# Performance work log

Hardware: AMD Instinct MI355X
Metric: run time of the kernel (lower is better)

## Reference

```python
import jax, jax.numpy as jnp
import numpy as np

B, N, E = 2, 5000, 160000
F_IN, HID, ED = 128, 128, 16
IN_EDGE = 2 * F_IN + 16 + ED  # source, target, radial(4*4), edge_attr


def _lin(k, fan_in, fan_out):
    return (jax.random.normal(k, (fan_in, fan_out), jnp.float32) / np.sqrt(fan_in)).astype(jnp.float32)


def setup_inputs() -> dict:
    key = jax.random.key(0)
    ks = jax.random.split(key, 16)
    h = jax.random.normal(ks[0], (B, N, F_IN), jnp.float32)
    coord = jax.random.normal(ks[1], (B, N, 4, 3), jnp.float32)
    edge_index = jax.random.randint(ks[2], (2, E), 0, N)
    edge_attr = jax.random.normal(ks[3], (E, ED), jnp.float32)
    return {
        "h": h, "coord": coord, "edge_index": edge_index, "edge_attr": edge_attr,
        # edge_mlp: Linear(IN_EDGE->HID), ReLU, Linear(HID->HID), ReLU
        "W_e1": _lin(ks[4], IN_EDGE, HID), "b_e1": jnp.zeros((HID,), jnp.float32),
        "W_e2": _lin(ks[5], HID, HID), "b_e2": jnp.zeros((HID,), jnp.float32),
        # node_mlp: Linear(HID+F_IN->HID), ReLU, Linear(HID->F_IN)
        "W_n1": _lin(ks[6], HID + F_IN, HID), "b_n1": jnp.zeros((HID,), jnp.float32),
        "W_n2": _lin(ks[7], HID, F_IN), "b_n2": jnp.zeros((F_IN,), jnp.float32),
        # coord_mlp: Linear(HID->HID), ReLU, Linear(HID->4, bias=False, xavier gain 0.001)
        "W_c1": _lin(ks[8], HID, HID), "b_c1": jnp.zeros((HID,), jnp.float32),
        "W_c2": _lin(ks[9], HID, 4) * 0.001,
    }


def reference(h, coord, edge_index, edge_attr,
              W_e1, b_e1, W_e2, b_e2,
              W_n1, b_n1, W_n2, b_n2,
              W_c1, b_c1, W_c2):
    row, col = edge_index[0], edge_index[1]
    coords_weight = 1.0
    n_nodes = h.shape[1]

    def single(h_b, coord_b):
        # coord2radial
        cd = coord_b[row] - coord_b[col]                                  # [E,4,3]
        prod = jnp.einsum('ejt,ekt->ejk', cd, cd).reshape(cd.shape[0], -1)  # [E,16]
        nrm = jnp.linalg.norm(prod, axis=-1, keepdims=True)
        radial = prod / jnp.maximum(nrm, 1e-12)                           # F.normalize
        # edge_model
        x = jnp.concatenate([h_b[row], h_b[col], radial, edge_attr], axis=-1)
        ef = jax.nn.relu(jax.nn.relu(x @ W_e1 + b_e1) @ W_e2 + b_e2)      # [E,HID]
        # coord_model: segment mean of cd * coord_mlp(ef)
        w = jax.nn.relu(ef @ W_c1 + b_c1) @ W_c2                          # [E,4]
        trans = cd * w[:, :, None]                                        # [E,4,3]
        agg_c = jax.ops.segment_sum(trans, row, num_segments=n_nodes)     # [N,4,3]
        cnt = jax.ops.segment_sum(jnp.ones((row.shape[0],), trans.dtype), row,
                                  num_segments=n_nodes)                   # [N]
        coord_new = coord_b + (agg_c / jnp.maximum(cnt, 1.0)[:, None, None]) * coords_weight
        # node_model (recurrent)
        agg_h = jax.ops.segment_sum(ef, row, num_segments=n_nodes)        # [N,HID]
        z = jnp.concatenate([h_b, agg_h], axis=-1)
        h_new = h_b + jax.nn.relu(z @ W_n1 + b_n1) @ W_n2 + b_n2
        return h_new, coord_new

    hs, coords = jax.vmap(single)(h, coord)
    return hs, coords
```

## Files before the change

### kernel.cpp

```cpp
#include <hip/hip_runtime.h>
#include <hip/hip_bf16.h>

#define B   2
#define NN_ 5000
#define NE_ 160000
#define F   128
#define HID 128
#define ED  16

typedef __bf16 bf16x8 __attribute__((ext_vector_type(8)));
typedef __bf16 bf16x4 __attribute__((ext_vector_type(4)));
typedef float  f32x4  __attribute__((ext_vector_type(4)));

#define MS  136
#define PS  40
#define EDG 64
#define ZS  264
#define HS  136
#define NPB2 32
#define NBUCKET 313

__global__ void pack_weights(const float* __restrict__ We1, const float* __restrict__ We2,
                             const float* __restrict__ Wc1, const float* __restrict__ Wc2,
                             const float* __restrict__ Wn1, const float* __restrict__ Wn2,
                             __bf16* __restrict__ pw1, __bf16* __restrict__ pw2,
                             __bf16* __restrict__ pwc1, __bf16* __restrict__ pwc2,
                             __bf16* __restrict__ pwn1, __bf16* __restrict__ pwn2,
                             float4* __restrict__ agg4, int* __restrict__ csr_cnt)
{
    int idx = blockIdx.x * 256 + threadIdx.x;
    const float* W; __bf16* P; int KT, Nr, local;
    if (idx < 36864)       { W = We1; P = pw1;  KT = 9; Nr = 128; local = idx; }
    else if (idx < 53248)  { W = We2; P = pw2;  KT = 4; Nr = 128; local = idx - 36864; }
    else if (idx < 69632)  { W = Wc1; P = pwc1; KT = 4; Nr = 128; local = idx - 53248; }
    else if (idx < 71680)  { W = Wc2; P = pwc2; KT = 4; Nr = 4;   local = idx - 69632; }
    else if (idx < 104448) { W = Wn1; P = pwn1; KT = 8; Nr = 128; local = idx - 71680; }
    else                   { W = Wn2; P = pwn2; KT = 4; Nr = 128; local = idx - 104448; }
    int j = local & 7, lane = (local >> 3) & 63, rest = local >> 9;
    int kt = rest % KT, nt = rest / KT;
    int k = kt * 32 + (lane >> 4) * 8 + j;
    int n = nt * 16 + (lane & 15);
    float v = (n < Nr) ? W[k * Nr + n] : 0.f;
    P[local] = (__bf16)v;

    float4 z4 = {0.f, 0.f, 0.f, 0.f};
    for (int i = idx; i < 350000; i += 120832) agg4[i] = z4;
    if (idx < NN_) csr_cnt[idx] = 0;
}

__global__ void hist_kernel(const int* __restrict__ ei, int* __restrict__ csr_cnt)
{
    int i = blockIdx.x * 256 + threadIdx.x;
    if (i < NE_) atomicAdd(&csr_cnt[ei[i]], 1);
}

__global__ void scan_kernel(const int* __restrict__ csr_cnt,
                            int* __restrict__ csr_off, int* __restrict__ csr_pos)
{
    __shared__ int part[256];
    const int t = threadIdx.x;
    int sum = 0;
    #pragma unroll
    for (int j = 0; j < 20; j++) {
        int idx = t * 20 + j;
        if (idx < NN_) sum += csr_cnt[idx];
    }
    part[t] = sum;
    __syncthreads();
    if (t == 0) {
        int run = 0;
        for (int i = 0; i < 256; i++) { int v = part[i]; part[i] = run; run += v; }
    }
    __syncthreads();
    int run = part[t];
    #pragma unroll
    for (int j = 0; j < 20; j++) {
        int idx = t * 20 + j;
        if (idx < NN_) { csr_off[idx] = run; csr_pos[idx] = run; run += csr_cnt[idx]; }
    }
    if (t == 0) csr_off[NN_] = NE_;
}

__global__ __launch_bounds__(512) void mid_kernel(
    const int* __restrict__ ei, const float* __restrict__ ea,
    int* __restrict__ csr_pos, int* __restrict__ bucket, __bf16* __restrict__ eas,
    const float* __restrict__ h, const __bf16* __restrict__ pw1,
    __bf16* __restrict__ pr, __bf16* __restrict__ pc)
{
    __shared__ __align__(16) __bf16 hs[128 * MS];
    const int t = threadIdx.x;

    if (blockIdx.x < NBUCKET) {
        int i = blockIdx.x * 512 + t;
        if (i < NE_) {
            int p = atomicAdd(&csr_pos[ei[i]], 1);
            bucket[p] = i;
            const float4* src = (const float4*)(ea + (size_t)i * ED);
            __bf16* dst = eas + (size_t)p * ED;
            #pragma unroll
            for (int j = 0; j < 4; j++) {
                float4 v = src[j];
                bf16x4 bv = {(__bf16)v.x, (__bf16)v.y, (__bf16)v.z, (__bf16)v.w};
                *(bf16x4*)&dst[j * 4] = bv;
            }
        }
        return;
    }

    const int bp = blockIdx.x - NBUCKET;
    const int b = bp / 40;
    const int n0 = (bp % 40) * 128;
    const int lane = t & 63, wave = t >> 6;
    const int quad = lane >> 4, c = lane & 15;

    #pragma unroll
    for (int it = 0; it < 8; it++) {
        int idx = it * 512 + t;
        int node = idx >> 5, ch = idx & 31;
        int gn = n0 + node;
        float4 v = (gn < NN_) ? *(const float4*)&h[((size_t)b * NN_ + gn) * F + ch * 4]
                              : (float4){0.f, 0.f, 0.f, 0.f};
        bf16x4 bv = {(__bf16)v.x, (__bf16)v.y, (__bf16)v.z, (__bf16)v.w};
        *(bf16x4*)&hs[node * MS + ch * 4] = bv;
    }
    __syncthreads();

    const bf16x8* pw1v = (const bf16x8*)pw1;
    f32x4 accr[8], accc[8];
    #pragma unroll
    for (int m = 0; m < 8; m++) { accr[m] = (f32x4){0,0,0,0}; accc[m] = (f32x4){0,0,0,0}; }
    for (int kt = 0; kt < 4; kt++) {
        bf16x8 wr = pw1v[(wave * 9 + kt) * 64 + lane];
        bf16x8 wc = pw1v[(wave * 9 + kt + 4) * 64 + lane];
        #pragma unroll
        for (int m = 0; m < 8; m++) {
            bf16x8 x = *(const bf16x8*)&hs[(m * 16 + c) * MS + kt * 32 + quad * 8];
            accr[m] = __builtin_amdgcn_mfma_f32_16x16x32_bf16(wr, x, accr[m], 0, 0, 0);
            accc[m] = __builtin_amdgcn_mfma_f32_16x16x32_bf16(wc, x, accc[m], 0, 0, 0);
        }
    }
    #pragma unroll
    for (int m = 0; m < 8; m++) {
        int gn = n0 + m * 16 + c;
        if (gn < NN_) {
            size_t base = ((size_t)b * NN_ + gn) * F + wave * 16 + quad * 4;
            bf16x4 orr = {(__bf16)accr[m][0], (__bf16)accr[m][1], (__bf16)accr[m][2], (__bf16)accr[m][3]};
            bf16x4 occ = {(__bf16)accc[m][0], (__bf16)accc[m][1], (__bf16)accc[m][2], (__bf16)accc[m][3]};
            *(bf16x4*)&pr[base] = orr;
            *(bf16x4*)&pc[base] = occ;
        }
    }
}

__global__ __launch_bounds__(256, 4) void edge_kernel(
    const __bf16* __restrict__ pr, const __bf16* __restrict__ pc,
    const float* __restrict__ coord,
    const int* __restrict__ ei, const __bf16* __restrict__ eas,
    const int* __restrict__ bucket,
    const float* __restrict__ be1, const float* __restrict__ be2,
    const float* __restrict__ bc1,
    const __bf16* __restrict__ pw1, const __bf16* __restrict__ pw2,
    const __bf16* __restrict__ pwc1, const __bf16* __restrict__ pwc2,
    float* __restrict__ agg_h, float* __restrict__ agg_c)
{
    __shared__ __align__(16) __bf16 buf1[EDG * MS];
    __shared__ __align__(16) __bf16 buf2[EDG * MS];
    __shared__ __bf16 cds[EDG][12];
    __shared__ int rs[EDG], cs[EDG];

    const int t = threadIdx.x;
    const int b = blockIdx.y;
    const int p0 = blockIdx.x * EDG;
    const int lane = t & 63, wave = t >> 6;
    const int quad = lane >> 4, c = lane & 15;

    if (t < EDG) {
        int eid = bucket[p0 + t];
        rs[t] = ei[eid]; cs[t] = ei[NE_ + eid];
    }
    __syncthreads();

    const __bf16* prb = pr + (size_t)b * NN_ * F;
    const __bf16* pcb = pc + (size_t)b * NN_ * F;
    #pragma unroll
    for (int it = 0; it < 4; it++) {
        int idx = it * 256 + t;
        int e = idx >> 4, ch = idx & 15;
        bf16x8 a = *(const bf16x8*)(prb + (size_t)rs[e] * F + ch * 8);
        bf16x8 v = *(const bf16x8*)(pcb + (size_t)cs[e] * F + ch * 8);
        bf16x8 o;
        #pragma unroll
        for (int j = 0; j < 8; j++) o[j] = (__bf16)((float)a[j] + (float)v[j]);
        *(bf16x8*)&buf1[e * MS + ch * 8] = o;
    }
    if (t < EDG) {
        int e = t;
        const float* cr = coord + ((size_t)b * NN_ + rs[e]) * 12;
        const float* cc = coord + ((size_t)b * NN_ + cs[e]) * 12;
        float cd[12];
        #pragma unroll
        for (int j = 0; j < 12; j++) { cd[j] = cr[j] - cc[j]; cds[e][j] = (__bf16)cd[j]; }
        float prod[16]; float ss = 0.f;
        #pragma unroll
        for (int j = 0; j < 4; j++)
            #pragma unroll
            for (int k = 0; k < 4; k++) {
                float p = cd[j*3]*cd[k*3] + cd[j*3+1]*cd[k*3+1] + cd[j*3+2]*cd[k*3+2];
                prod[j*4 + k] = p; ss += p * p;
            }
        float inv = 1.0f / fmaxf(sqrtf(ss), 1e-12f);
        #pragma unroll
        for (int j = 0; j < 16; j++) buf2[e * PS + j] = (__bf16)(prod[j] * inv);
        const uint4* ep = (const uint4*)(eas + (size_t)(p0 + e) * 16);
        *(uint4*)&buf2[e * PS + 16] = ep[0];
        *(uint4*)&buf2[e * PS + 24] = ep[1];
    }
    __syncthreads();

    const bf16x8* pw1v  = (const bf16x8*)pw1;
    const bf16x8* pw2v  = (const bf16x8*)pw2;
    const bf16x8* pwc1v = (const bf16x8*)pwc1;
    const bf16x8* pwc2v = (const bf16x8*)pwc2;

    f32x4 acc1[4][2];
    #pragma unroll
    for (int m = 0; m < 4; m++)
        #pragma unroll
        for (int n = 0; n < 2; n++) acc1[m][n] = (f32x4){0,0,0,0};
    {
        bf16x8 x1[4];
        #pragma unroll
        for (int m = 0; m < 4; m++)
            x1[m] = *(const bf16x8*)&buf2[(m*16 + c) * PS + quad*8];
        #pragma unroll
        for (int n = 0; n < 2; n++) {
            bf16x8 w = pw1v[((2*wave + n)*9 + 8)*64 + lane];
            #pragma unroll
            for (int m = 0; m < 4; m++)
                acc1[m][n] = __builtin_amdgcn_mfma_f32_16x16x32_bf16(w, x1[m], acc1[m][n], 0, 0, 0);
        }
    }
    #pragma unroll
    for (int n = 0; n < 2; n++) {
        int nt = 2*wave + n;
        float4 bb = *(const float4*)&be1[nt*16 + quad*4];
        #pragma unroll
        for (int m = 0; m < 4; m++) {
            int row = m*16 + c;
            bf16x4 p = *(const bf16x4*)&buf1[row * MS + nt*16 + quad*4];
            bf16x4 o = { (__bf16)fmaxf(acc1[m][n][0] + (float)p[0] + bb.x, 0.f),
                         (__bf16)fmaxf(acc1[m][n][1] + (float)p[1] + bb.y, 0.f),
                         (__bf16)fmaxf(acc1[m][n][2] + (float)p[2] + bb.z, 0.f),
                         (__bf16)fmaxf(acc1[m][n][3] + (float)p[3] + bb.w, 0.f) };
            *(bf16x4*)&buf1[row * MS + nt*16 + quad*4] = o;
        }
    }
    __syncthreads();

    f32x4 acc2[4][2];
    #pragma unroll
    for (int m = 0; m < 4; m++)
        #pragma unroll
        for (int n = 0; n < 2; n++) acc2[m][n] = (f32x4){0,0,0,0};
    for (int kt = 0; kt < 4; kt++) {
        bf16x8 x[4];
        #pragma unroll
        for (int m = 0; m < 4; m++)
            x[m] = *(const bf16x8*)&buf1[(m*16 + c) * MS + kt*32 + quad*8];
        #pragma unroll
        for (int n = 0; n < 2; n++) {
            bf16x8 w = pw2v[((2*wave + n)*4 + kt)*64 + lane];
            #pragma unroll
            for (int m = 0; m < 4; m++)
                acc2[m][n] = __builtin_amdgcn_mfma_f32_16x16x32_bf16(w, x[m], acc2[m][n], 0, 0, 0);
        }
    }
    #pragma unroll
    for (int n = 0; n < 2; n++) {
        int nt = 2*wave + n;
        float4 bb = *(const float4*)&be2[nt*16 + quad*4];
        #pragma unroll
        for (int m = 0; m < 4; m++) {
            int row = m*16 + c;
            bf16x4 o = { (__bf16)fmaxf(acc2[m][n][0] + bb.x, 0.f),
                         (__bf16)fmaxf(acc2[m][n][1] + bb.y, 0.f),
                         (__bf16)fmaxf(acc2[m][n][2] + bb.z, 0.f),
                         (__bf16)fmaxf(acc2[m][n][3] + bb.w, 0.f) };
            *(bf16x4*)&buf2[row * MS + nt*16 + quad*4] = o;
        }
    }
    __syncthreads();

    f32x4 acc3[4][2];
    #pragma unroll
    for (int m = 0; m < 4; m++)
        #pragma unroll
        for (int n = 0; n < 2; n++) acc3[m][n] = (f32x4){0,0,0,0};
    for (int kt = 0; kt < 4; kt++) {
        bf16x8 x[4];
        #pragma unroll
        for (int m = 0; m < 4; m++)
            x[m] = *(const bf16x8*)&buf2[(m*16 + c) * MS + kt*32 + quad*8];
        #pragma unroll
        for (int n = 0; n < 2; n++) {
            bf16x8 w = pwc1v[((2*wave + n)*4 + kt)*64 + lane];
            #pragma unroll
            for (int m = 0; m < 4; m++)
                acc3[m][n] = __builtin_amdgcn_mfma_f32_16x16x32_bf16(w, x[m], acc3[m][n], 0, 0, 0);
        }
    }
    #pragma unroll
    for (int n = 0; n < 2; n++) {
        int nt = 2*wave + n;
        float4 bb = *(const float4*)&bc1[nt*16 + quad*4];
        #pragma unroll
        for (int m = 0; m < 4; m++) {
            int row = m*16 + c;
            bf16x4 o = { (__bf16)fmaxf(acc3[m][n][0] + bb.x, 0.f),
                         (__bf16)fmaxf(acc3[m][n][1] + bb.y, 0.f),
                         (__bf16)fmaxf(acc3[m][n][2] + bb.z, 0.f),
                         (__bf16)fmaxf(acc3[m][n][3] + bb.w, 0.f) };
            *(bf16x4*)&buf1[row * MS + nt*16 + quad*4] = o;
        }
    }
    __syncthreads();

    f32x4 accw = (f32x4){0,0,0,0};
    for (int kt = 0; kt < 4; kt++) {
        bf16x8 x = *(const bf16x8*)&buf1[(wave*16 + c) * MS + kt*32 + quad*8];
        accw = __builtin_amdgcn_mfma_f32_16x16x32_bf16(pwc2v[kt*64 + lane], x, accw, 0, 0, 0);
    }
    if (quad == 0) {
        int e = wave*16 + c;
        #pragma unroll
        for (int j = 0; j < 12; j++)
            cds[e][j] = (__bf16)((float)cds[e][j] * accw[j/3]);
    }
    __syncthreads();

    {
        float* aggh_b = agg_h + (size_t)b * NN_ * HID;
        const int cp = t & 63;
        const int seg = t >> 6;
        float r0 = 0.f, r1 = 0.f;
        int cur = rs[seg * 16];
        for (int e = seg * 16; e < seg * 16 + 16; e++) {
            int r = rs[e];
            unsigned u = *(const unsigned*)&buf2[e * MS + cp * 2];
            float v0 = __uint_as_float(u << 16);
            float v1 = __uint_as_float(u & 0xffff0000u);
            if (r != cur) {
                atomicAdd(&aggh_b[(size_t)cur * HID + cp*2],     r0);
                atomicAdd(&aggh_b[(size_t)cur * HID + cp*2 + 1], r1);
                r0 = r1 = 0.f; cur = r;
            }
            r0 += v0; r1 += v1;
        }
        atomicAdd(&aggh_b[(size_t)cur * HID + cp*2],     r0);
        atomicAdd(&aggh_b[(size_t)cur * HID + cp*2 + 1], r1);
    }
    if (t < 48) {
        float* aggc_b = agg_c + (size_t)b * NN_ * 12;
        const int j = t % 12, q = t / 12;
        float run = 0.f;
        int cur = rs[q * 16];
        for (int e = q * 16; e < q * 16 + 16; e++) {
            int r = rs[e];
            float v = (float)cds[e][j];
            if (r != cur) {
                atomicAdd(&aggc_b[(size_t)cur * 12 + j], run);
                run = 0.f; cur = r;
            }
            run += v;
        }
        atomicAdd(&aggc_b[(size_t)cur * 12 + j], run);
    }
}

__global__ __launch_bounds__(256) void node_kernel(
    const float* __restrict__ h, const float* __restrict__ agg_h,
    const float* __restrict__ agg_c, const float* __restrict__ coord,
    const int* __restrict__ csr_off,
    const __bf16* __restrict__ pwn1, const float* __restrict__ bn1,
    const __bf16* __restrict__ pwn2, const float* __restrict__ bn2,
    float* __restrict__ out_h, float* __restrict__ out_c)
{
    __shared__ __align__(16) __bf16 zs[NPB2 * ZS];
    __shared__ __align__(16) __bf16 h1s[NPB2 * HS];
    const int t = threadIdx.x;
    const int b = blockIdx.y;
    const int n0 = blockIdx.x * NPB2;
    const int lane = t & 63, wave = t >> 6;
    const int quad = lane >> 4, c = lane & 15;

    #pragma unroll
    for (int it = 0; it < 8; it++) {
        int idx = it * 256 + t;
        int node = idx >> 6, ch = idx & 63;
        int gn = n0 + node;
        float4 v = (float4){0.f, 0.f, 0.f, 0.f};
        if (gn < NN_) {
            const float* src = (ch < 32) ? &h[((size_t)b * NN_ + gn) * F + ch * 4]
                                         : &agg_h[((size_t)b * NN_ + gn) * HID + (ch - 32) * 4];
            v = *(const float4*)src;
        }
        bf16x4 bv = {(__bf16)v.x, (__bf16)v.y, (__bf16)v.z, (__bf16)v.w};
        *(bf16x4*)&zs[node * ZS + ch * 4] = bv;
    }
    __syncthreads();

    const bf16x8* w1v = (const bf16x8*)pwn1;
    const bf16x8* w2v = (const bf16x8*)pwn2;
    f32x4 a1[2][2];
    #pragma unroll
    for (int m = 0; m < 2; m++)
        #pragma unroll
        for (int n = 0; n < 2; n++) a1[m][n] = (f32x4){0,0,0,0};
    for (int kt = 0; kt < 8; kt++) {
        bf16x8 x[2];
        #pragma unroll
        for (int m = 0; m < 2; m++)
            x[m] = *(const bf16x8*)&zs[(m*16 + c) * ZS + kt*32 + quad*8];
        #pragma unroll
        for (int n = 0; n < 2; n++) {
            bf16x8 w = w1v[((2*wave + n)*8 + kt)*64 + lane];
            #pragma unroll
            for (int m = 0; m < 2; m++)
                a1[m][n] = __builtin_amdgcn_mfma_f32_16x16x32_bf16(w, x[m], a1[m][n], 0, 0, 0);
        }
    }
    __syncthreads();
    #pragma unroll
    for (int n = 0; n < 2; n++) {
        int nt = 2*wave + n;
        float4 bb = *(const float4*)&bn1[nt*16 + quad*4];
        #pragma unroll
        for (int m = 0; m < 2; m++) {
            bf16x4 o = { (__bf16)fmaxf(a1[m][n][0] + bb.x, 0.f),
                         (__bf16)fmaxf(a1[m][n][1] + bb.y, 0.f),
                         (__bf16)fmaxf(a1[m][n][2] + bb.z, 0.f),
                         (__bf16)fmaxf(a1[m][n][3] + bb.w, 0.f) };
            *(bf16x4*)&h1s[(m*16 + c) * HS + nt*16 + quad*4] = o;
        }
    }
    __syncthreads();

    f32x4 a2[2][2];
    #pragma unroll
    for (int m = 0; m < 2; m++)
        #pragma unroll
        for (int n = 0; n < 2; n++) a2[m][n] = (f32x4){0,0,0,0};
    for (int kt = 0; kt < 4; kt++) {
        bf16x8 x[2];
        #pragma unroll
        for (int m = 0; m < 2; m++)
            x[m] = *(const bf16x8*)&h1s[(m*16 + c) * HS + kt*32 + quad*8];
        #pragma unroll
        for (int n = 0; n < 2; n++) {
            bf16x8 w = w2v[((2*wave + n)*4 + kt)*64 + lane];
            #pragma unroll
            for (int m = 0; m < 2; m++)
                a2[m][n] = __builtin_amdgcn_mfma_f32_16x16x32_bf16(w, x[m], a2[m][n], 0, 0, 0);
        }
    }
    float* os = (float*)zs;
    #pragma unroll
    for (int n = 0; n < 2; n++) {
        int nt = 2*wave + n;
        float4 bb = *(const float4*)&bn2[nt*16 + quad*4];
        #pragma unroll
        for (int m = 0; m < 2; m++) {
            f32x4 o = { a2[m][n][0] + bb.x, a2[m][n][1] + bb.y,
                        a2[m][n][2] + bb.z, a2[m][n][3] + bb.w };
            *(f32x4*)&os[(m*16 + c) * 132 + nt*16 + quad*4] = o;
        }
    }
    __syncthreads();

    #pragma unroll
    for (int it = 0; it < 4; it++) {
        int idx = it * 256 + t;
        int node = idx >> 5, ch = idx & 31;
        int gn = n0 + node;
        if (gn < NN_) {
            size_t gb = ((size_t)b * NN_ + gn) * F + ch * 4;
            float4 hres = *(const float4*)&h[gb];
            float4 acc = *(const float4*)&os[node * 132 + ch * 4];
            float4 o = { hres.x + acc.x, hres.y + acc.y, hres.z + acc.z, hres.w + acc.w };
            *(float4*)&out_h[gb] = o;
        }
    }
    for (int idx = t; idx < NPB2 * 12; idx += 256) {
        int node = idx / 12, j = idx % 12;
        int gn = n0 + node;
        if (gn < NN_) {
            float deg = (float)(csr_off[gn + 1] - csr_off[gn]);
            size_t ci = ((size_t)b * NN_ + gn) * 12 + j;
            out_c[ci] = coord[ci] + agg_c[ci] / fmaxf(deg, 1.0f);
        }
    }
}

extern "C" void kernel_launch(void* const* d_in, const int* in_sizes, int n_in,
                              void* d_out, int out_size, void* d_ws, size_t ws_size,
                              hipStream_t stream) {
    const float* h     = (const float*)d_in[0];
    const float* coord = (const float*)d_in[1];
    const int*   ei    = (const int*)d_in[2];
    const float* ea    = (const float*)d_in[3];
    const float* We1   = (const float*)d_in[4];
    const float* be1   = (const float*)d_in[5];
    const float* We2   = (const float*)d_in[6];
    const float* be2   = (const float*)d_in[7];
    const float* Wn1   = (const float*)d_in[8];
    const float* bn1   = (const float*)d_in[9];
    const float* Wn2   = (const float*)d_in[10];
    const float* bn2   = (const float*)d_in[11];
    const float* Wc1   = (const float*)d_in[12];
    const float* bc1   = (const float*)d_in[13];
    const float* Wc2   = (const float*)d_in[14];

    float* out_h = (float*)d_out;
    float* out_c = out_h + (size_t)B * NN_ * F;

    unsigned char* base = (unsigned char*)d_ws;
    __bf16* pw1  = (__bf16*)base;
    __bf16* pw2  = pw1 + 36864;
    __bf16* pwc1 = pw2 + 16384;
    __bf16* pwc2 = pwc1 + 16384;
    __bf16* pwn1 = pwc2 + 2048;
    __bf16* pwn2 = pwn1 + 32768;
    unsigned char* dyn = base + 241664;

    int* csr_cnt = (int*)(dyn);
    int* csr_off = (int*)(dyn + 20000);
    int* csr_pos = (int*)(dyn + 40016);
    int* bucket  = (int*)(dyn + 60016);
    float* agg_h = (float*)(dyn + 700016);
    float* agg_c = agg_h + (size_t)B * NN_ * HID;
    __bf16* pr   = (__bf16*)(agg_c + (size_t)B * NN_ * 12);
    __bf16* pc   = pr + (size_t)B * NN_ * F;
    __bf16* eas  = pc + (size_t)B * NN_ * F;

    pack_weights<<<472, 256, 0, stream>>>(We1, We2, Wc1, Wc2, Wn1, Wn2,
                                          pw1, pw2, pwc1, pwc2, pwn1, pwn2,
                                          (float4*)agg_h, csr_cnt);

    hist_kernel<<<625, 256, 0, stream>>>(ei, csr_cnt);
    scan_kernel<<<1, 256, 0, stream>>>(csr_cnt, csr_off, csr_pos);

    mid_kernel<<<NBUCKET + 80, 512, 0, stream>>>(ei, ea, csr_pos, bucket, eas,
                                                 h, pw1, pr, pc);

    dim3 eg(NE_ / EDG, B);
    edge_kernel<<<eg, 256, 0, stream>>>(pr, pc, coord, ei, eas, bucket, be1, be2, bc1,
                                        pw1, pw2, pwc1, pwc2, agg_h, agg_c);

    dim3 ng((NN_ + NPB2 - 1) / NPB2, B);
    node_kernel<<<ng, 256, 0, stream>>>(h, agg_h, agg_c, coord, csr_off,
                                        pwn1, bn1, pwn2, bn2, out_h, out_c);
}
```

Before: 204.1 us.

## Merge setup kernels into one cooperative kernel; gather projections into registers

The four setup launches (weight packing, histogram, scan, bucket plus node projection) become one cooperative kernel of 256 blocks that uses grid-wide syncs between phases, and the scan becomes a parallel Hillis-Steele pass. The goal is to remove launch gaps and tail idling between small kernels. In the edge kernel, the projected row and column features are now loaded straight into registers in MFMA output layout, so the shared-memory staging pass and its barrier are gone. An extra __syncthreads is added, and the grid syncs plus the fixed grid size could limit parallelism in the bucket and projection phases.

```diff
diff --git a/kernel.cpp b/kernel.cpp
--- a/kernel.cpp
+++ b/kernel.cpp
@@ -1,5 +1,8 @@
 #include <hip/hip_runtime.h>
 #include <hip/hip_bf16.h>
+#include <hip/hip_cooperative_groups.h>
+
+namespace cg = cooperative_groups;
 
 #define B   2
 #define NN_ 5000
@@ -18,136 +21,133 @@
 #define ZS  264
 #define HS  136
 #define NPB2 32
-#define NBUCKET 313
-
-__global__ void pack_weights(const float* __restrict__ We1, const float* __restrict__ We2,
-                             const float* __restrict__ Wc1, const float* __restrict__ Wc2,
-                             const float* __restrict__ Wn1, const float* __restrict__ Wn2,
-                             __bf16* __restrict__ pw1, __bf16* __restrict__ pw2,
-                             __bf16* __restrict__ pwc1, __bf16* __restrict__ pwc2,
-                             __bf16* __restrict__ pwn1, __bf16* __restrict__ pwn2,
-                             float4* __restrict__ agg4, int* __restrict__ csr_cnt)
-{
-    int idx = blockIdx.x * 256 + threadIdx.x;
-    const float* W; __bf16* P; int KT, Nr, local;
-    if (idx < 36864)       { W = We1; P = pw1;  KT = 9; Nr = 128; local = idx; }
-    else if (idx < 53248)  { W = We2; P = pw2;  KT = 4; Nr = 128; local = idx - 36864; }
-    else if (idx < 69632)  { W = Wc1; P = pwc1; KT = 4; Nr = 128; local = idx - 53248; }
-    else if (idx < 71680)  { W = Wc2; P = pwc2; KT = 4; Nr = 4;   local = idx - 69632; }
-    else if (idx < 104448) { W = Wn1; P = pwn1; KT = 8; Nr = 128; local = idx - 71680; }
-    else                   { W = Wn2; P = pwn2; KT = 4; Nr = 128; local = idx - 104448; }
-    int j = local & 7, lane = (local >> 3) & 63, rest = local >> 9;
-    int kt = rest % KT, nt = rest / KT;
-    int k = kt * 32 + (lane >> 4) * 8 + j;
-    int n = nt * 16 + (lane & 15);
-    float v = (n < Nr) ? W[k * Nr + n] : 0.f;
-    P[local] = (__bf16)v;
-
-    float4 z4 = {0.f, 0.f, 0.f, 0.f};
-    for (int i = idx; i < 350000; i += 120832) agg4[i] = z4;
-    if (idx < NN_) csr_cnt[idx] = 0;
-}
-
-__global__ void hist_kernel(const int* __restrict__ ei, int* __restrict__ csr_cnt)
-{
-    int i = blockIdx.x * 256 + threadIdx.x;
-    if (i < NE_) atomicAdd(&csr_cnt[ei[i]], 1);
-}
-
-__global__ void scan_kernel(const int* __restrict__ csr_cnt,
-                            int* __restrict__ csr_off, int* __restrict__ csr_pos)
-{
-    __shared__ int part[256];
-    const int t = threadIdx.x;
-    int sum = 0;
-    #pragma unroll
-    for (int j = 0; j < 20; j++) {
-        int idx = t * 20 + j;
-        if (idx < NN_) sum += csr_cnt[idx];
-    }
-    part[t] = sum;
-    __syncthreads();
-    if (t == 0) {
-        int run = 0;
-        for (int i = 0; i < 256; i++) { int v = part[i]; part[i] = run; run += v; }
-    }
-    __syncthreads();
-    int run = part[t];
-    #pragma unroll
-    for (int j = 0; j < 20; j++) {
-        int idx = t * 20 + j;
-        if (idx < NN_) { csr_off[idx] = run; csr_pos[idx] = run; run += csr_cnt[idx]; }
-    }
-    if (t == 0) csr_off[NN_] = NE_;
-}
-
-__global__ __launch_bounds__(512) void mid_kernel(
+
+__global__ __launch_bounds__(512) void setup_kernel(
+    const float* __restrict__ We1, const float* __restrict__ We2,
+    const float* __restrict__ Wc1, const float* __restrict__ Wc2,
+    const float* __restrict__ Wn1, const float* __restrict__ Wn2,
     const int* __restrict__ ei, const float* __restrict__ ea,
-    int* __restrict__ csr_pos, int* __restrict__ bucket, __bf16* __restrict__ eas,
-    const float* __restrict__ h, const __bf16* __restrict__ pw1,
+    const float* __restrict__ h,
+    __bf16* __restrict__ pw1, __bf16* __restrict__ pw2,
+    __bf16* __restrict__ pwc1, __bf16* __restrict__ pwc2,
+    __bf16* __restrict__ pwn1, __bf16* __restrict__ pwn2,
+    float4* __restrict__ agg4, int* __restrict__ csr_cnt,
+    int* __restrict__ csr_off, int* __restrict__ csr_pos,
+    int* __restrict__ bucket, __bf16* __restrict__ eas,
     __bf16* __restrict__ pr, __bf16* __restrict__ pc)
 {
     __shared__ __align__(16) __bf16 hs[128 * MS];
+    __shared__ int part[512];
+    cg::grid_group grid = cg::this_grid();
     const int t = threadIdx.x;
-
-    if (blockIdx.x < NBUCKET) {
-        int i = blockIdx.x * 512 + t;
-        if (i < NE_) {
-            int p = atomicAdd(&csr_pos[ei[i]], 1);
-            bucket[p] = i;
-            const float4* src = (const float4*)(ea + (size_t)i * ED);
-            __bf16* dst = eas + (size_t)p * ED;
-            #pragma unroll
-            for (int j = 0; j < 4; j++) {
-                float4 v = src[j];
-                bf16x4 bv = {(__bf16)v.x, (__bf16)v.y, (__bf16)v.z, (__bf16)v.w};
-                *(bf16x4*)&dst[j * 4] = bv;
+    const int gid = blockIdx.x * 512 + t;
+
+    if (gid < 120832) {
+        int idx = gid;
+        const float* W; __bf16* P; int KT, Nr, local;
+        if (idx < 36864)       { W = We1; P = pw1;  KT = 9; Nr = 128; local = idx; }
+        else if (idx < 53248)  { W = We2; P = pw2;  KT = 4; Nr = 128; local = idx - 36864; }
+        else if (idx < 69632)  { W = Wc1; P = pwc1; KT = 4; Nr = 128; local = idx - 53248; }
+        else if (idx < 71680)  { W = Wc2; P = pwc2; KT = 4; Nr = 4;   local = idx - 69632; }
+        else if (idx < 104448) { W = Wn1; P = pwn1; KT = 8; Nr = 128; local = idx - 71680; }
+        else                   { W = Wn2; P = pwn2; KT = 4; Nr = 128; local = idx - 104448; }
+        int j = local & 7, lane = (local >> 3) & 63, rest = local >> 9;
+        int kt = rest % KT, nt = rest / KT;
+        int k = kt * 32 + (lane >> 4) * 8 + j;
+        int n = nt * 16 + (lane & 15);
+        float v = (n < Nr) ? W[k * Nr + n] : 0.f;
+        P[local] = (__bf16)v;
+    }
+    {
+        float4 z4 = {0.f, 0.f, 0.f, 0.f};
+        for (int i = gid; i < 350000; i += 131072) agg4[i] = z4;
+    }
+    if (gid < NN_) csr_cnt[gid] = 0;
+    grid.sync();
+
+    for (int i = gid; i < NE_; i += 131072) atomicAdd(&csr_cnt[ei[i]], 1);
+    grid.sync();
+
+    if (blockIdx.x == 0) {
+        int sum = 0;
+        #pragma unroll
+        for (int j = 0; j < 10; j++) {
+            int idx = t * 10 + j;
+            if (idx < NN_) sum += csr_cnt[idx];
+        }
+        part[t] = sum;
+        __syncthreads();
+        for (int off = 1; off < 512; off <<= 1) {
+            int v = (t >= off) ? part[t - off] : 0;
+            __syncthreads();
+            part[t] += v;
+            __syncthreads();
+        }
+        int run = part[t] - sum;
+        #pragma unroll
+        for (int j = 0; j < 10; j++) {
+            int idx = t * 10 + j;
+            if (idx < NN_) { csr_off[idx] = run; csr_pos[idx] = run; run += csr_cnt[idx]; }
+        }
+        if (t == 0) csr_off[NN_] = NE_;
+    }
+    grid.sync();
+
+    for (int i = gid; i < NE_; i += 131072) {
+        int p = atomicAdd(&csr_pos[ei[i]], 1);
+        bucket[p] = i;
+        const float4* src = (const float4*)(ea + (size_t)i * ED);
+        __bf16* dst = eas + (size_t)p * ED;
+        #pragma unroll
+        for (int j = 0; j < 4; j++) {
+            float4 v = src[j];
+            bf16x4 bv = {(__bf16)v.x, (__bf16)v.y, (__bf16)v.z, (__bf16)v.w};
+            *(bf16x4*)&dst[j * 4] = bv;
+        }
+    }
+    if (blockIdx.x >= 176) {
+        const int bp = blockIdx.x - 176;
+        const int b = bp / 40;
+        const int n0 = (bp % 40) * 128;
+        const int lane = t & 63, wave = t >> 6;
+        const int quad = lane >> 4, c = lane & 15;
+
+        #pragma unroll
+        for (int it = 0; it < 8; it++) {
+            int idx = it * 512 + t;
+            int node = idx >> 5, ch = idx & 31;
+            int gn = n0 + node;
+            float4 v = (gn < NN_) ? *(const float4*)&h[((size_t)b * NN_ + gn) * F + ch * 4]
+                                  : (float4){0.f, 0.f, 0.f, 0.f};
+            bf16x4 bv = {(__bf16)v.x, (__bf16)v.y, (__bf16)v.z, (__bf16)v.w};
+            *(bf16x4*)&hs[node * MS + ch * 4] = bv;
+        }
+        __syncthreads();
+
+        const bf16x8* pw1v = (const bf16x8*)pw1;
+        f32x4 accr[8], accc[8];
+        #pragma unroll
+        for (int m = 0; m < 8; m++) { accr[m] = (f32x4){0,0,0,0}; accc[m] = (f32x4){0,0,0,0}; }
+        for (int kt = 0; kt < 4; kt++) {
+            bf16x8 wr = pw1v[(wave * 9 + kt) * 64 + lane];
+            bf16x8 wc = pw1v[(wave * 9 + kt + 4) * 64 + lane];
+            #pragma unroll
+            for (int m = 0; m < 8; m++) {
+                bf16x8 x = *(const bf16x8*)&hs[(m * 16 + c) * MS + kt * 32 + quad * 8];
+                accr[m] = __builtin_amdgcn_mfma_f32_16x16x32_bf16(wr, x, accr[m], 0, 0, 0);
+                accc[m] = __builtin_amdgcn_mfma_f32_16x16x32_bf16(wc, x, accc[m], 0, 0, 0);
             }
         }
-        return;
-    }
-
-    const int bp = blockIdx.x - NBUCKET;
-    const int b = bp / 40;
-    const int n0 = (bp % 40) * 128;
-    const int lane = t & 63, wave = t >> 6;
-    const int quad = lane >> 4, c = lane & 15;
-
-    #pragma unroll
-    for (int it = 0; it < 8; it++) {
-        int idx = it * 512 + t;
-        int node = idx >> 5, ch = idx & 31;
-        int gn = n0 + node;
-        float4 v = (gn < NN_) ? *(const float4*)&h[((size_t)b * NN_ + gn) * F + ch * 4]
-                              : (float4){0.f, 0.f, 0.f, 0.f};
-        bf16x4 bv = {(__bf16)v.x, (__bf16)v.y, (__bf16)v.z, (__bf16)v.w};
-        *(bf16x4*)&hs[node * MS + ch * 4] = bv;
-    }
-    __syncthreads();
-
-    const bf16x8* pw1v = (const bf16x8*)pw1;
-    f32x4 accr[8], accc[8];
-    #pragma unroll
-    for (int m = 0; m < 8; m++) { accr[m] = (f32x4){0,0,0,0}; accc[m] = (f32x4){0,0,0,0}; }
-    for (int kt = 0; kt < 4; kt++) {
-        bf16x8 wr = pw1v[(wave * 9 + kt) * 64 + lane];
-        bf16x8 wc = pw1v[(wave * 9 + kt + 4) * 64 + lane];
         #pragma unroll
         for (int m = 0; m < 8; m++) {
-            bf16x8 x = *(const bf16x8*)&hs[(m * 16 + c) * MS + kt * 32 + quad * 8];
-            accr[m] = __builtin_amdgcn_mfma_f32_16x16x32_bf16(wr, x, accr[m], 0, 0, 0);
-            accc[m] = __builtin_amdgcn_mfma_f32_16x16x32_bf16(wc, x, accc[m], 0, 0, 0);
-        }
-    }
-    #pragma unroll
-    for (int m = 0; m < 8; m++) {
-        int gn = n0 + m * 16 + c;
-        if (gn < NN_) {
-            size_t base = ((size_t)b * NN_ + gn) * F + wave * 16 + quad * 4;
-            bf16x4 orr = {(__bf16)accr[m][0], (__bf16)accr[m][1], (__bf16)accr[m][2], (__bf16)accr[m][3]};
-            bf16x4 occ = {(__bf16)accc[m][0], (__bf16)accc[m][1], (__bf16)accc[m][2], (__bf16)accc[m][3]};
-            *(bf16x4*)&pr[base] = orr;
-            *(bf16x4*)&pc[base] = occ;
+            int gn = n0 + m * 16 + c;
+            if (gn < NN_) {
+                size_t base = ((size_t)b * NN_ + gn) * F + wave * 16 + quad * 4;
+                bf16x4 orr = {(__bf16)accr[m][0], (__bf16)accr[m][1], (__bf16)accr[m][2], (__bf16)accr[m][3]};
+                bf16x4 occ = {(__bf16)accc[m][0], (__bf16)accc[m][1], (__bf16)accc[m][2], (__bf16)accc[m][3]};
+                *(bf16x4*)&pr[base] = orr;
+                *(bf16x4*)&pc[base] = occ;
+            }
         }
     }
 }
@@ -175,28 +175,12 @@
     const int quad = lane >> 4, c = lane & 15;
 
     if (t < EDG) {
-        int eid = bucket[p0 + t];
-        rs[t] = ei[eid]; cs[t] = ei[NE_ + eid];
-    }
-    __syncthreads();
-
-    const __bf16* prb = pr + (size_t)b * NN_ * F;
-    const __bf16* pcb = pc + (size_t)b * NN_ * F;
-    #pragma unroll
-    for (int it = 0; it < 4; it++) {
-        int idx = it * 256 + t;
-        int e = idx >> 4, ch = idx & 15;
-        bf16x8 a = *(const bf16x8*)(prb + (size_t)rs[e] * F + ch * 8);
-        bf16x8 v = *(const bf16x8*)(pcb + (size_t)cs[e] * F + ch * 8);
-        bf16x8 o;
-        #pragma unroll
-        for (int j = 0; j < 8; j++) o[j] = (__bf16)((float)a[j] + (float)v[j]);
-        *(bf16x8*)&buf1[e * MS + ch * 8] = o;
-    }
-    if (t < EDG) {
         int e = t;
-        const float* cr = coord + ((size_t)b * NN_ + rs[e]) * 12;
-        const float* cc = coord + ((size_t)b * NN_ + cs[e]) * 12;
+        int eid = bucket[p0 + e];
+        int r = ei[eid], cl = ei[NE_ + eid];
+        rs[e] = r; cs[e] = cl;
+        const float* cr = coord + ((size_t)b * NN_ + r) * 12;
+        const float* cc = coord + ((size_t)b * NN_ + cl) * 12;
         float cd[12];
         #pragma unroll
         for (int j = 0; j < 12; j++) { cd[j] = cr[j] - cc[j]; cds[e][j] = (__bf16)cd[j]; }
@@ -221,6 +205,20 @@
     const bf16x8* pw2v  = (const bf16x8*)pw2;
     const bf16x8* pwc1v = (const bf16x8*)pwc1;
     const bf16x8* pwc2v = (const bf16x8*)pwc2;
+    const __bf16* prb = pr + (size_t)b * NN_ * F;
+    const __bf16* pcb = pc + (size_t)b * NN_ * F;
+
+    bf16x4 pgr[2][4], pgc[2][4];
+    #pragma unroll
+    for (int n = 0; n < 2; n++) {
+        int fo = (2*wave + n)*16 + quad*4;
+        #pragma unroll
+        for (int m = 0; m < 4; m++) {
+            int e = m*16 + c;
+            pgr[n][m] = *(const bf16x4*)(prb + (size_t)rs[e] * F + fo);
+            pgc[n][m] = *(const bf16x4*)(pcb + (size_t)cs[e] * F + fo);
+        }
+    }
 
     f32x4 acc1[4][2];
     #pragma unroll
@@ -247,11 +245,10 @@
         #pragma unroll
         for (int m = 0; m < 4; m++) {
             int row = m*16 + c;
-            bf16x4 p = *(const bf16x4*)&buf1[row * MS + nt*16 + quad*4];
-            bf16x4 o = { (__bf16)fmaxf(acc1[m][n][0] + (float)p[0] + bb.x, 0.f),
-                         (__bf16)fmaxf(acc1[m][n][1] + (float)p[1] + bb.y, 0.f),
-                         (__bf16)fmaxf(acc1[m][n][2] + (float)p[2] + bb.z, 0.f),
-                         (__bf16)fmaxf(acc1[m][n][3] + (float)p[3] + bb.w, 0.f) };
+            bf16x4 o = { (__bf16)fmaxf(acc1[m][n][0] + (float)pgr[n][m][0] + (float)pgc[n][m][0] + bb.x, 0.f),
+                         (__bf16)fmaxf(acc1[m][n][1] + (float)pgr[n][m][1] + (float)pgc[n][m][1] + bb.y, 0.f),
+                         (__bf16)fmaxf(acc1[m][n][2] + (float)pgr[n][m][2] + (float)pgc[n][m][2] + bb.z, 0.f),
+                         (__bf16)fmaxf(acc1[m][n][3] + (float)pgr[n][m][3] + (float)pgc[n][m][3] + bb.w, 0.f) };
             *(bf16x4*)&buf1[row * MS + nt*16 + quad*4] = o;
         }
     }
@@ -275,6 +272,7 @@
                 acc2[m][n] = __builtin_amdgcn_mfma_f32_16x16x32_bf16(w, x[m], acc2[m][n], 0, 0, 0);
         }
     }
+    __syncthreads();
     #pragma unroll
     for (int n = 0; n < 2; n++) {
         int nt = 2*wave + n;
@@ -542,15 +540,15 @@
     __bf16* pc   = pr + (size_t)B * NN_ * F;
     __bf16* eas  = pc + (size_t)B * NN_ * F;
 
-    pack_weights<<<472, 256, 0, stream>>>(We1, We2, Wc1, Wc2, Wn1, Wn2,
-                                          pw1, pw2, pwc1, pwc2, pwn1, pwn2,
-                                          (float4*)agg_h, csr_cnt);
-
-    hist_kernel<<<625, 256, 0, stream>>>(ei, csr_cnt);
-    scan_kernel<<<1, 256, 0, stream>>>(csr_cnt, csr_off, csr_pos);
-
-    mid_kernel<<<NBUCKET + 80, 512, 0, stream>>>(ei, ea, csr_pos, bucket, eas,
-                                                 h, pw1, pr, pc);
+    float4* agg4 = (float4*)agg_h;
+    void* args[] = {
+        (void*)&We1, (void*)&We2, (void*)&Wc1, (void*)&Wc2, (void*)&Wn1, (void*)&Wn2,
+        (void*)&ei, (void*)&ea, (void*)&h,
+        (void*)&pw1, (void*)&pw2, (void*)&pwc1, (void*)&pwc2, (void*)&pwn1, (void*)&pwn2,
+        (void*)&agg4, (void*)&csr_cnt, (void*)&csr_off, (void*)&csr_pos,
+        (void*)&bucket, (void*)&eas, (void*)&pr, (void*)&pc
+    };
+    hipLaunchCooperativeKernel((void*)setup_kernel, dim3(256), dim3(512), args, 0, stream);
 
     dim3 eg(NE_ / EDG, B);
     edge_kernel<<<eg, 256, 0, stream>>>(pr, pc, coord, ei, eas, bucket, be1, be2, bc1,
```

Measured after the change: 318.0 us. 1.56x slower.

## Gather node projections directly into registers and widen edge segments for scatter

Applied to the files above, without the earlier changes.

The precomputed row/col projections are now gathered straight into registers in the MFMA output layout instead of being staged through shared memory. This removes one shared-memory round trip and a barrier before the first GEMM. The scatter phase now gives each thread one column over 32 edges instead of two columns over 16 edges, so consecutive same-row edges merge into fewer atomics. In exchange the gathers are narrower (8-byte) and less coalesced, register pressure rises, and a barrier is added after the second GEMM because buf2 is reused.

```diff
diff --git a/kernel.cpp b/kernel.cpp
--- a/kernel.cpp
+++ b/kernel.cpp
@@ -175,28 +175,12 @@
     const int quad = lane >> 4, c = lane & 15;
 
     if (t < EDG) {
-        int eid = bucket[p0 + t];
-        rs[t] = ei[eid]; cs[t] = ei[NE_ + eid];
-    }
-    __syncthreads();
-
-    const __bf16* prb = pr + (size_t)b * NN_ * F;
-    const __bf16* pcb = pc + (size_t)b * NN_ * F;
-    #pragma unroll
-    for (int it = 0; it < 4; it++) {
-        int idx = it * 256 + t;
-        int e = idx >> 4, ch = idx & 15;
-        bf16x8 a = *(const bf16x8*)(prb + (size_t)rs[e] * F + ch * 8);
-        bf16x8 v = *(const bf16x8*)(pcb + (size_t)cs[e] * F + ch * 8);
-        bf16x8 o;
-        #pragma unroll
-        for (int j = 0; j < 8; j++) o[j] = (__bf16)((float)a[j] + (float)v[j]);
-        *(bf16x8*)&buf1[e * MS + ch * 8] = o;
-    }
-    if (t < EDG) {
         int e = t;
-        const float* cr = coord + ((size_t)b * NN_ + rs[e]) * 12;
-        const float* cc = coord + ((size_t)b * NN_ + cs[e]) * 12;
+        int eid = bucket[p0 + e];
+        int r = ei[eid], cl = ei[NE_ + eid];
+        rs[e] = r; cs[e] = cl;
+        const float* cr = coord + ((size_t)b * NN_ + r) * 12;
+        const float* cc = coord + ((size_t)b * NN_ + cl) * 12;
         float cd[12];
         #pragma unroll
         for (int j = 0; j < 12; j++) { cd[j] = cr[j] - cc[j]; cds[e][j] = (__bf16)cd[j]; }
@@ -221,6 +205,20 @@
     const bf16x8* pw2v  = (const bf16x8*)pw2;
     const bf16x8* pwc1v = (const bf16x8*)pwc1;
     const bf16x8* pwc2v = (const bf16x8*)pwc2;
+    const __bf16* prb = pr + (size_t)b * NN_ * F;
+    const __bf16* pcb = pc + (size_t)b * NN_ * F;
+
+    bf16x4 pgr[2][4], pgc[2][4];
+    #pragma unroll
+    for (int n = 0; n < 2; n++) {
+        int fo = (2*wave + n)*16 + quad*4;
+        #pragma unroll
+        for (int m = 0; m < 4; m++) {
+            int e = m*16 + c;
+            pgr[n][m] = *(const bf16x4*)(prb + (size_t)rs[e] * F + fo);
+            pgc[n][m] = *(const bf16x4*)(pcb + (size_t)cs[e] * F + fo);
+        }
+    }
 
     f32x4 acc1[4][2];
     #pragma unroll
@@ -247,11 +245,10 @@
         #pragma unroll
         for (int m = 0; m < 4; m++) {
             int row = m*16 + c;
-            bf16x4 p = *(const bf16x4*)&buf1[row * MS + nt*16 + quad*4];
-            bf16x4 o = { (__bf16)fmaxf(acc1[m][n][0] + (float)p[0] + bb.x, 0.f),
-                         (__bf16)fmaxf(acc1[m][n][1] + (float)p[1] + bb.y, 0.f),
-                         (__bf16)fmaxf(acc1[m][n][2] + (float)p[2] + bb.z, 0.f),
-                         (__bf16)fmaxf(acc1[m][n][3] + (float)p[3] + bb.w, 0.f) };
+            bf16x4 o = { (__bf16)fmaxf(acc1[m][n][0] + (float)pgr[n][m][0] + (float)pgc[n][m][0] + bb.x, 0.f),
+                         (__bf16)fmaxf(acc1[m][n][1] + (float)pgr[n][m][1] + (float)pgc[n][m][1] + bb.y, 0.f),
+                         (__bf16)fmaxf(acc1[m][n][2] + (float)pgr[n][m][2] + (float)pgc[n][m][2] + bb.z, 0.f),
+                         (__bf16)fmaxf(acc1[m][n][3] + (float)pgr[n][m][3] + (float)pgc[n][m][3] + bb.w, 0.f) };
             *(bf16x4*)&buf1[row * MS + nt*16 + quad*4] = o;
         }
     }
@@ -275,6 +272,7 @@
                 acc2[m][n] = __builtin_amdgcn_mfma_f32_16x16x32_bf16(w, x[m], acc2[m][n], 0, 0, 0);
         }
     }
+    __syncthreads();
     #pragma unroll
     for (int n = 0; n < 2; n++) {
         int nt = 2*wave + n;
@@ -340,31 +338,26 @@
 
     {
         float* aggh_b = agg_h + (size_t)b * NN_ * HID;
-        const int cp = t & 63;
-        const int seg = t >> 6;
-        float r0 = 0.f, r1 = 0.f;
-        int cur = rs[seg * 16];
-        for (int e = seg * 16; e < seg * 16 + 16; e++) {
+        const int col = t & 127, seg = t >> 7;
+        float run = 0.f;
+        int cur = rs[seg * 32];
+        for (int e = seg * 32; e < seg * 32 + 32; e++) {
             int r = rs[e];
-            unsigned u = *(const unsigned*)&buf2[e * MS + cp * 2];
-            float v0 = __uint_as_float(u << 16);
-            float v1 = __uint_as_float(u & 0xffff0000u);
+            float v = (float)buf2[e * MS + col];
             if (r != cur) {
-                atomicAdd(&aggh_b[(size_t)cur * HID + cp*2],     r0);
-                atomicAdd(&aggh_b[(size_t)cur * HID + cp*2 + 1], r1);
-                r0 = r1 = 0.f; cur = r;
+                atomicAdd(&aggh_b[(size_t)cur * HID + col], run);
+                run = 0.f; cur = r;
             }
-            r0 += v0; r1 += v1;
-        }
-        atomicAdd(&aggh_b[(size_t)cur * HID + cp*2],     r0);
-        atomicAdd(&aggh_b[(size_t)cur * HID + cp*2 + 1], r1);
-    }
-    if (t < 48) {
+            run += v;
+        }
+        atomicAdd(&aggh_b[(size_t)cur * HID + col], run);
+    }
+    if (t < 24) {
         float* aggc_b = agg_c + (size_t)b * NN_ * 12;
         const int j = t % 12, q = t / 12;
         float run = 0.f;
-        int cur = rs[q * 16];
-        for (int e = q * 16; e < q * 16 + 16; e++) {
+        int cur = rs[q * 32];
+        for (int e = q * 32; e < q * 32 + 32; e++) {
             int r = rs[e];
             float v = (float)cds[e][j];
             if (r != cur) {
```

New measurement: 215.1 us. 1.05x slower.
